# Performance work log

Measured on AMD Instinct MI355X. Metric: run time of the kernel, lower is better.

Reference implementation:

```python
import jax, jax.numpy as jnp
import numpy as np
from jax import lax

C = 256          # hidden_channels
K_ITERS = 3      # num_iterations

def _conv(x, w, b, stride=1, pad='SAME'):
    y = lax.conv_general_dilated(x, w, (stride, stride), pad,
                                 dimension_numbers=('NCHW', 'OIHW', 'NCHW'))
    return y + b[None, :, None, None]

def setup_inputs() -> dict:
    key = jax.random.key(0)
    ks = jax.random.split(key, 16)
    B, N, H, W = 1, 3, 384, 384
    def p(k, sh, scale=None):
        if scale is None:
            scale = 1.0 / np.sqrt(np.prod(sh[1:]))
        return jax.random.normal(k, sh, jnp.float32) * scale
    z = lambda: jnp.zeros((C,), jnp.float32)
    return {
        'frames': jax.random.normal(ks[0], (B, N, 3, H, W), jnp.float32),
        'backbone_w': p(ks[1], (C, 3, 8, 8)), 'backbone_b': z(),
        'W_intra': p(ks[2], (C, C), scale=1.0 / C),
        'W_inter': p(ks[3], (C, C), scale=1.0 / C),
        'gate_w': p(ks[4], (C, C, 1, 1)), 'gate_b': z(),
        'Wz': p(ks[5], (C, 2 * C, 3, 3)), 'bz': z(),
        'Wr': p(ks[6], (C, 2 * C, 3, 3)), 'br': z(),
        'Wh': p(ks[7], (C, 2 * C, 3, 3)), 'bh': z(),
        'ro_w1': p(ks[8], (C, 2 * C, 3, 3)), 'ro_b1': z(),
        'ro_w2': p(ks[9], (1, C, 3, 3)), 'ro_b2': jnp.zeros((1,), jnp.float32),
    }

def _forward(frames, backbone_w, backbone_b, W_intra, W_inter, gate_w, gate_b,
             Wz, bz, Wr, br, Wh, bh, ro_w1, ro_b1, ro_w2, ro_b2):
    B, N, _, H, W = frames.shape
    x = frames.reshape(B * N, 3, H, W)
    # backbone: stride-8 conv + ReLU -> node embeddings v (B*N, C, Hf, Wf)
    v = jax.nn.relu(_conv(x, backbone_w, backbone_b, stride=8, pad='VALID'))
    Hf, Wf = v.shape[2], v.shape[3]
    P = Hf * Wf
    v = v.reshape(B, N, C, Hf, Wf)
    h = v
    idx = jnp.arange(N)
    for _ in range(K_ITERS):
        hp = h.reshape(B, N, C, P).transpose(0, 1, 3, 2)      # (B,N,P,C)
        # inter attention e_ij = h_i W h_j^T over all ordered pairs
        t = jnp.einsum('bipc,cd->bipd', hp, W_inter)
        e = jnp.einsum('bipd,bjqd->bijpq', t, hp)              # (B,N,N,P,P)
        # intra (loop-edge) attention on the diagonal, own weight
        ti = jnp.einsum('bipc,cd->bipd', hp, W_intra)
        e_intra = jnp.einsum('bipd,biqd->bipq', ti, hp)        # (B,N,P,P)
        e = e.at[:, idx, idx].set(e_intra)
        attn = jax.nn.softmax(e, axis=-1)
        m = jnp.einsum('bijpq,bjqc->bijpc', attn, hp)          # msg j->i (B,N,N,P,C)
        m = m.transpose(0, 1, 2, 4, 3).reshape(B * N * N, C, Hf, Wf)
        # gated aggregation: sigmoid(1x1 conv) gate, sum over senders j
        g = jax.nn.sigmoid(_conv(m, gate_w, gate_b))
        magg = (g * m).reshape(B, N, N, C, Hf, Wf).sum(axis=2).reshape(B * N, C, Hf, Wf)
        # ConvGRU update
        hflat = h.reshape(B * N, C, Hf, Wf)
        mh = jnp.concatenate([magg, hflat], axis=1)
        zg = jax.nn.sigmoid(_conv(mh, Wz, bz))
        rg = jax.nn.sigmoid(_conv(mh, Wr, br))
        hc = jnp.tanh(_conv(jnp.concatenate([magg, rg * hflat], axis=1), Wh, bh))
        h = ((1.0 - zg) * hflat + zg * hc).reshape(B, N, C, Hf, Wf)
    # read-out on concat(h, v)
    cat = jnp.concatenate([h, v], axis=2).reshape(B * N, 2 * C, Hf, Wf)
    y = jax.nn.relu(_conv(cat, ro_w1, ro_b1))
    masks = _conv(y, ro_w2, ro_b2)
    return masks.reshape(B, N, 1, Hf, Wf)

def reference(frames, backbone_w, backbone_b, W_intra, W_inter, gate_w, gate_b,
              Wz, bz, Wr, br, Wh, bh, ro_w1, ro_b1, ro_w2, ro_b2):
    return _forward(frames, backbone_w, backbone_b, W_intra, W_inter, gate_w, gate_b,
                    Wz, bz, Wr, br, Wh, bh, ro_w1, ro_b1, ro_w2, ro_b2)
```

## Files before the change

### kernel.cpp

```cpp
#include <hip/hip_runtime.h>
#include <hip/hip_bf16.h>
#include <math.h>

#define PIX 2304
#define CCH 256
#define CP  589824
#define NCP 1769472
#define KC  4608
#define PADR 2512

typedef __hip_bfloat16 bf16;
typedef __attribute__((ext_vector_type(8))) short bf16x8;
typedef __attribute__((ext_vector_type(4))) float f32x4;

__device__ __forceinline__ float sigmoidf_(float x){ return 1.f/(1.f+__expf(-x)); }

__device__ __forceinline__ void gl_lds16(const bf16* g, bf16* lds){
    __builtin_amdgcn_global_load_lds(
        (const __attribute__((address_space(1))) void*)g,
        (__attribute__((address_space(3))) void*)lds, 16, 0, 0);
}
#define FENCE() asm volatile("" ::: "memory")

__device__ __forceinline__ float bperm_f(int srcLane, float v){
    return __int_as_float(__builtin_amdgcn_ds_bpermute(srcLane<<2, __float_as_int(v)));
}
__device__ __forceinline__ unsigned packbf(float lo, float hi){
    bf16 a = __float2bfloat16(lo), b = __float2bfloat16(hi);
    return (unsigned)(*(unsigned short*)&a) | ((unsigned)(*(unsigned short*)&b)<<16);
}

__global__ __launch_bounds__(512) void fattn_k(
    const bf16* __restrict__ T, const bf16* __restrict__ Ti,
    const bf16* __restrict__ Khp, const bf16* __restrict__ Vcp,
    bf16* __restrict__ Ob)
{
    __shared__ bf16 Ks[2][64*256];
    __shared__ bf16 Vs[2][256*64];
    __shared__ unsigned Ps[8][512];
    const int z = blockIdx.z, i = z/3, j = z%3;
    const bf16* Q  = ((i==j)? Ti : T) + (long)i*CP;
    const bf16* Kp = Khp + (long)j*CP;
    const bf16* Vp = Vcp + (long)j*CP;
    const int tid = threadIdx.x, l = tid & 63, w = tid >> 6;
    const int g = l>>4, m = l&15;
    const int q0 = blockIdx.x*128;

    bf16x8 qf[8];
    {
        const bf16* qr = Q + (long)(q0 + w*16 + m)*256 + g*8;
        #pragma unroll
        for (int ks=0; ks<8; ++ks) qf[ks] = *(const bf16x8*)(qr + ks*32);
    }
    f32x4 oacc[16];
    #pragma unroll
    for (int nf=0; nf<16; ++nf) oacc[nf] = (f32x4){0.f,0.f,0.f,0.f};
    float mrun = -3e38f;
    float lrun = 0.f;

    auto stage = [&](int buf, int t){
        const int kq = t*64;
        #pragma unroll
        for (int u=0; u<4; ++u){
            int idx = u*512 + tid;
            int rr = idx>>5, cc = idx&31;
            gl_lds16(Kp + (long)(kq+rr)*256 + ((cc ^ (rr&7))<<3),
                     &Ks[buf][(u*512 + (tid & ~63))*8]);
        }
        #pragma unroll
        for (int u=0; u<4; ++u){
            int idx = u*512 + tid;
            int rr = idx>>3, cc = idx&7;
            gl_lds16(Vp + (long)rr*2304 + kq + ((cc ^ (rr&7))<<3),
                     &Vs[buf][(u*512 + (tid & ~63))*8]);
        }
    };

    stage(0, 0);
    int cur = 0;
    char* pw = (char*)&Ps[w][0];
    for (int t=0; t<36; ++t){
        if (t+1 < 36){
            stage(cur^1, t+1);
            asm volatile("s_waitcnt vmcnt(8)" ::: "memory");
        } else {
            asm volatile("s_waitcnt vmcnt(0)" ::: "memory");
        }
        __builtin_amdgcn_s_barrier();
        FENCE();

        f32x4 sacc[4];
        #pragma unroll
        for (int nf=0; nf<4; ++nf) sacc[nf] = (f32x4){0.f,0.f,0.f,0.f};
        __builtin_amdgcn_s_setprio(1);
        #pragma unroll
        for (int ks=0; ks<8; ++ks){
            #pragma unroll
            for (int nf=0; nf<4; ++nf){
                int row = nf*16 + m;
                int phys = (ks*4 + g) ^ (row&7);
                bf16x8 kf = *(const bf16x8*)&Ks[cur][row*256 + phys*8];
                sacc[nf] = __builtin_amdgcn_mfma_f32_16x16x32_bf16(kf, qf[ks], sacc[nf], 0,0,0);
            }
        }
        __builtin_amdgcn_s_setprio(0);

        float pmax = -3e38f;
        #pragma unroll
        for (int nf=0; nf<4; ++nf)
            #pragma unroll
            for (int r=0; r<4; ++r) pmax = fmaxf(pmax, sacc[nf][r]);
        pmax = fmaxf(pmax, __shfl_xor(pmax, 16));
        pmax = fmaxf(pmax, __shfl_xor(pmax, 32));
        if (!__all(pmax - mrun <= 8.f)){
            float mn = fmaxf(mrun, pmax);
            float al = __expf(mrun - mn);
            mrun = mn;
            lrun *= al;
            float ar[4];
            #pragma unroll
            for (int r=0; r<4; ++r) ar[r] = bperm_f((l & 48) | (g*4 + r), al);
            #pragma unroll
            for (int nf=0; nf<16; ++nf)
                #pragma unroll
                for (int r=0; r<4; ++r) oacc[nf][r] *= ar[r];
        }
        float rs = 0.f;
        unsigned pk[4][2];
        #pragma unroll
        for (int nf=0; nf<4; ++nf){
            float p0 = __expf(sacc[nf][0] - mrun);
            float p1 = __expf(sacc[nf][1] - mrun);
            float p2 = __expf(sacc[nf][2] - mrun);
            float p3 = __expf(sacc[nf][3] - mrun);
            rs += (p0+p1) + (p2+p3);
            pk[nf][0] = packbf(p0, p1);
            pk[nf][1] = packbf(p2, p3);
        }
        rs += __shfl_xor(rs, 16);
        rs += __shfl_xor(rs, 32);
        lrun += rs;
        #pragma unroll
        for (int nf=0; nf<4; ++nf)
            #pragma unroll
            for (int s=0; s<2; ++s){
                int ba = m*128 + ((nf*32 + g*8 + s*4) ^ ((m&7)<<4));
                *(unsigned*)(pw + ba) = pk[nf][s];
            }
        asm volatile("s_waitcnt lgkmcnt(0)" ::: "memory");
        __builtin_amdgcn_sched_barrier(0);
        __builtin_amdgcn_s_setprio(1);
        #pragma unroll
        for (int ks2=0; ks2<2; ++ks2){
            bf16x8 pa = *(const bf16x8*)(pw + m*128 + ((ks2*64 + g*16) ^ ((m&7)<<4)));
            #pragma unroll
            for (int nf=0; nf<16; ++nf){
                int row = nf*16 + m;
                int phys = (ks2*4 + g) ^ (row&7);
                bf16x8 bv = *(const bf16x8*)&Vs[cur][row*64 + phys*8];
                oacc[nf] = __builtin_amdgcn_mfma_f32_16x16x32_bf16(pa, bv, oacc[nf], 0,0,0);
            }
        }
        __builtin_amdgcn_s_setprio(0);
        FENCE();
        __builtin_amdgcn_s_barrier();
        FENCE();
        cur ^= 1;
    }

    float linv = 1.f / lrun;
    float li[4];
    #pragma unroll
    for (int r=0; r<4; ++r) li[r] = bperm_f((l & 48) | (g*4 + r), linv);
    bf16* ob = Ob + (long)z*CP;
    const int prow0 = q0 + w*16 + g*4;
    #pragma unroll
    for (int nf=0; nf<16; ++nf){
        int c = nf*16 + m;
        #pragma unroll
        for (int r=0; r<4; ++r)
            ob[(long)(prow0+r)*256 + c] = __float2bfloat16(oacc[nf][r]*li[r]);
    }
}

template<int EPI, int BN>
__global__ __launch_bounds__(256) void mgemm_k(
    const bf16* __restrict__ A0, const bf16* __restrict__ A1, int diagz,
    const bf16* __restrict__ B,
    float* __restrict__ o0, bf16* __restrict__ ob,
    const bf16* __restrict__ aux, const float* __restrict__ bias0,
    int M, int N, int lda, int ldb, int ldc, int auxld,
    long bsA, long bsB, long bsC, long bsAux,
    int nzJ, int Ksub, long bsKc)
{
    __shared__ bf16 As[2][128*64];
    __shared__ bf16 Bs[2][BN*64];
    const int z = blockIdx.z;
    const int jz = z % nzJ, kc = z / nzJ;
    const bf16* Ap = ((jz==diagz)?A1:A0) + jz*bsA + (long)blockIdx.x*128*lda;
    const bf16* Bp = B + jz*bsB + (long)blockIdx.y*BN*ldb;
    const int tid = threadIdx.x, l = tid & 63;
    const int wvu = tid & ~63;
    const int wr = tid>>7, wc = (tid>>6)&1;
    constexpr int NF = BN/32;
    f32x4 acc[4][NF];
    #pragma unroll
    for (int i=0;i<4;++i)
        #pragma unroll
        for (int j=0;j<NF;++j) acc[i][j] = (f32x4){0.f,0.f,0.f,0.f};

    auto stage = [&](int buf, int kb){
        #pragma unroll
        for (int u=0;u<4;++u){
            int idx = u*256 + tid;
            int row = idx>>3, g = (idx&7) ^ (row&7);
            gl_lds16(Ap + (long)row*lda + kb + g*8, &As[buf][(u*256+wvu)*8]);
        }
        #pragma unroll
        for (int u=0;u<BN/32;++u){
            int idx = u*256 + tid;
            int row = idx>>3, g = (idx&7) ^ (row&7);
            gl_lds16(Bp + (long)row*ldb + kb + g*8, &Bs[buf][(u*256+wvu)*8]);
        }
    };

    const int kbeg = kc*Ksub;
    const int nk = Ksub >> 6;
    stage(0, kbeg);
    int cur = 0;
    for (int t=0; t<nk; ++t){
        if (t+1 < nk){
            stage(cur^1, kbeg + (t+1)*64);
            if constexpr (BN==64) asm volatile("s_waitcnt vmcnt(6)" ::: "memory");
            else                  asm volatile("s_waitcnt vmcnt(8)" ::: "memory");
        } else {
            asm volatile("s_waitcnt vmcnt(0)" ::: "memory");
        }
        __builtin_amdgcn_s_barrier();
        FENCE();
        #pragma unroll
        for (int ks=0; ks<64; ks+=32){
            bf16x8 af[4], bfr[NF];
            #pragma unroll
            for (int i=0;i<4;++i){
                int row = wr*64 + i*16 + (l&15);
                af[i] = *(const bf16x8*)&As[cur][row*64 + ((((ks>>3)+(l>>4)) ^ (row&7))<<3)];
            }
            #pragma unroll
            for (int j=0;j<NF;++j){
                int row = wc*(BN/2) + j*16 + (l&15);
                bfr[j] = *(const bf16x8*)&Bs[cur][row*64 + ((((ks>>3)+(l>>4)) ^ (row&7))<<3)];
            }
            #pragma unroll
            for (int i=0;i<4;++i)
                #pragma unroll
                for (int j=0;j<NF;++j)
                    acc[i][j] = __builtin_amdgcn_mfma_f32_16x16x32_bf16(af[i], bfr[j], acc[i][j], 0,0,0);
        }
        FENCE();
        __builtin_amdgcn_s_barrier();
        FENCE();
        cur ^= 1;
    }

    const int mb = blockIdx.x*128 + wr*64, nb = blockIdx.y*BN + wc*(BN/2);
    #pragma unroll
    for (int i=0;i<4;++i)
        #pragma unroll
        for (int j=0;j<NF;++j){
            int gm0 = mb + i*16 + ((l>>4)<<2);
            int gn  = nb + j*16 + (l&15);
            #pragma unroll
            for (int r=0;r<4;++r){
                int gm = gm0 + r;
                float vacc = acc[i][j][r];
                if (EPI==0){
                    ob[jz*bsC + (long)gm*ldc + gn] = __float2bfloat16(vacc);
                } else {
                    float g = sigmoidf_(vacc + bias0[gm]);
                    float mv = __bfloat162float(aux[jz*bsAux + (long)gn*auxld + gm]);
                    o0[jz*bsC + (long)gm*ldc + gn] = g*mv;
                }
            }
        }
}

__global__ __launch_bounds__(256) void cgemm2_k(
    const bf16* __restrict__ inpad, const bf16* __restrict__ W,
    float* __restrict__ part, int N)
{
    __shared__ bf16 As[2][128*64];
    __shared__ bf16 Bs[2][64*64];
    const int tid = threadIdx.x, l = tid & 63, wvu = tid & ~63;
    const int wr = tid>>7, wc = (tid>>6)&1;
    const int bx = blockIdx.x, by = blockIdx.y, kc = blockIdx.z;
    const int img = bx/18, m0 = (bx - img*18)*128;
    const bf16* Ab = inpad + (long)img*PADR*512;
    const bf16* Bb = W + (long)by*64*KC;
    f32x4 acc[4][2];
    #pragma unroll
    for (int i=0;i<4;++i){ acc[i][0]=(f32x4){0,0,0,0}; acc[i][1]=(f32x4){0,0,0,0}; }

    auto stageA = [&](int buf, int k0){
        int tap = k0 >> 9, ci0 = k0 & 511;
        int dy = tap/3, dx = tap - 3*dy;
        int shift = (dy-1)*50 + (dx-1);
        #pragma unroll
        for (int u=0;u<4;++u){
            int idx = u*256 + tid;
            int row = idx>>3;
            int om = m0 + row;
            int prow = om + 2*(om/48) + 51 + shift;
            int g = (idx&7) ^ (row&7);
            gl_lds16(Ab + (long)prow*512 + ci0 + g*8, &As[buf][(u*256+wvu)*8]);
        }
    };
    auto stageB = [&](int buf, int k0){
        #pragma unroll
        for (int u=0;u<2;++u){
            int idx = u*256 + tid;
            int row = idx>>3;
            int g = (idx&7) ^ (row&7);
            gl_lds16(Bb + (long)row*KC + k0 + g*8, &Bs[buf][(u*256+wvu)*8]);
        }
    };

    const int kbeg = kc*2304;
    stageA(0, kbeg); stageB(0, kbeg);
    int cur = 0;
    for (int t=0; t<36; ++t){
        if (t+1 < 36){
            stageA(cur^1, kbeg+(t+1)*64); stageB(cur^1, kbeg+(t+1)*64);
            asm volatile("s_waitcnt vmcnt(6)" ::: "memory");
        } else {
            asm volatile("s_waitcnt vmcnt(0)" ::: "memory");
        }
        __builtin_amdgcn_s_barrier();
        FENCE();
        #pragma unroll
        for (int ks=0; ks<64; ks+=32){
            bf16x8 af[4], bfr[2];
            #pragma unroll
            for (int i=0;i<4;++i){
                int row = wr*64 + i*16 + (l&15);
                af[i] = *(const bf16x8*)&As[cur][row*64 + ((((ks>>3)+(l>>4)) ^ (row&7))<<3)];
            }
            #pragma unroll
            for (int j=0;j<2;++j){
                int row = wc*32 + j*16 + (l&15);
                bfr[j] = *(const bf16x8*)&Bs[cur][row*64 + ((((ks>>3)+(l>>4)) ^ (row&7))<<3)];
            }
            #pragma unroll
            for (int i=0;i<4;++i)
                #pragma unroll
                for (int j=0;j<2;++j)
                    acc[i][j] = __builtin_amdgcn_mfma_f32_16x16x32_bf16(af[i], bfr[j], acc[i][j], 0,0,0);
        }
        FENCE();
        __builtin_amdgcn_s_barrier();
        FENCE();
        cur ^= 1;
    }

    float* pbase = part + (long)kc*N*6912 + (long)img*2304;
    #pragma unroll
    for (int i=0;i<4;++i)
        #pragma unroll
        for (int j=0;j<2;++j){
            int gm0 = m0 + wr*64 + i*16 + ((l>>4)<<2);
            int gn  = by*64 + wc*32 + j*16 + (l&15);
            *(f32x4*)&pbase[(long)gn*6912 + gm0] = acc[i][j];
        }
}

template<int ACT, int DUAL>
__global__ __launch_bounds__(256) void cred_k(const float* __restrict__ part,
        const float* __restrict__ b0, const float* __restrict__ b1,
        float* __restrict__ o0, float* __restrict__ o1,
        const float* __restrict__ hmul, int N)
{
    int id = blockIdx.x*256 + threadIdx.x;
    int c = id / 6912, g = id - c*6912;
    int img = g / 2304, p = g - img*2304;
    float v = part[id] + part[id + (long)N*6912];
    if (DUAL && c >= 256){
        int co = c - 256;
        long oidx = (long)img*CP + (long)co*PIX + p;
        o1[oidx] = sigmoidf_(v + b1[co]) * hmul[oidx];
    } else {
        float r = v + b0[c];
        if (ACT==1) r = sigmoidf_(r);
        else if (ACT==2) r = tanhf(r);
        else r = fmaxf(r, 0.f);
        o0[(long)img*CP + (long)c*PIX + p] = r;
    }
}

__global__ __launch_bounds__(256) void padtr_k(const float* __restrict__ src,
        bf16* __restrict__ dst, int cofs)
{
    __shared__ float tile[64][65];
    const int img = blockIdx.z, p0 = blockIdx.x*64, c0 = blockIdx.y*64;
    const int t = threadIdx.x, tx = t&63, tq = t>>6;
    const float* s = src + (long)img*CP;
    #pragma unroll
    for (int u=0;u<16;++u){
        int r = tq + u*4;
        tile[r][tx] = s[(long)(c0+r)*PIX + p0 + tx];
    }
    __syncthreads();
    bf16* d = dst + (long)img*PADR*512 + cofs + c0;
    #pragma unroll
    for (int u=0;u<16;++u){
        int pl = tq + u*4;
        int p = p0 + pl;
        int prow = p + 2*(p/48) + 51;
        d[(long)prow*512 + tx] = __float2bfloat16(tile[tx][pl]);
    }
}

__global__ __launch_bounds__(256) void convw_k(const float* __restrict__ src,
        bf16* __restrict__ dst, int total)
{
    int idx = blockIdx.x*256 + threadIdx.x;
    if (idx >= total) return;
    int co = idx / KC, r = idx - co*KC;
    int tap = r >> 9, ci = r & 511;
    dst[idx] = __float2bfloat16(src[(long)co*KC + ci*9 + tap]);
}

__global__ __launch_bounds__(256) void prep_h_k(const float* __restrict__ h,
        bf16* __restrict__ hcp, bf16* __restrict__ hp)
{
    __shared__ float tile[64][65];
    const int i = blockIdx.z, p0 = blockIdx.x*64, c0 = blockIdx.y*64;
    const int t = threadIdx.x, tx = t&63, tq = t>>6;
    const float* src = h + (long)i*CP;
    #pragma unroll
    for (int s=0;s<16;++s){
        int r = tq + s*4;
        float v = src[(long)(c0+r)*PIX + p0 + tx];
        tile[r][tx] = v;
        hcp[(long)i*CP + (long)(c0+r)*PIX + p0 + tx] = __float2bfloat16(v);
    }
    __syncthreads();
    #pragma unroll
    for (int s=0;s<16;++s){
        int r = tq + s*4;
        hp[(long)i*CP + (long)(p0+r)*256 + c0 + tx] = __float2bfloat16(tile[tx][r]);
    }
}

__global__ __launch_bounds__(256) void convert_w_k(const float* __restrict__ wint,
    const float* __restrict__ wintra, const float* __restrict__ gw, bf16* __restrict__ o)
{
    int t = blockIdx.x*256 + threadIdx.x;
    int d = t >> 8, c = t & 255;
    o[t]          = __float2bfloat16(wint[c*256 + d]);
    o[65536 + t]  = __float2bfloat16(wintra[c*256 + d]);
    o[131072 + t] = __float2bfloat16(gw[t]);
}

__global__ __launch_bounds__(256) void gatesum_k(const float* __restrict__ g, float* __restrict__ out)
{
    int x = blockIdx.x*256 + threadIdx.x;
    int i = blockIdx.y;
    const float* gi = g + (long)i*3*CP;
    float4 a = ((const float4*)gi)[x];
    float4 b = ((const float4*)gi)[x + CP/4];
    float4 c = ((const float4*)gi)[x + CP/2];
    float4 r; r.x=a.x+b.x+c.x; r.y=a.y+b.y+c.y; r.z=a.z+b.z+c.z; r.w=a.w+b.w+c.w;
    ((float4*)(out + (long)i*CP))[x] = r;
}

__global__ __launch_bounds__(256) void backbone_k(
    const float* __restrict__ frames, const float* __restrict__ W,
    const float* __restrict__ bias, float* __restrict__ v, float* __restrict__ h)
{
    __shared__ float wl[3*64*4];
    const int n = blockIdx.z, o0 = blockIdx.y * 4;
    const int p = blockIdx.x * 256 + threadIdx.x;
    const int y = p / 48, x = p % 48;
    for (int e = threadIdx.x; e < 768; e += 256) {
        int o_sel = e / 192, rem = e % 192, ci = rem / 64, k = rem % 64;
        wl[(ci*64 + k)*4 + o_sel] = W[((long)(o0 + o_sel)*3 + ci)*64 + k];
    }
    __syncthreads();
    float acc[4] = {0.f,0.f,0.f,0.f};
    for (int ci = 0; ci < 3; ++ci) {
        const float* src = frames + (((long)n*3 + ci)*384) * 384;
        #pragma unroll
        for (int k = 0; k < 64; ++k) {
            int ky = k >> 3, kx = k & 7;
            float iv = src[(8*y + ky)*384 + 8*x + kx];
            float4 w = ((const float4*)wl)[ci*64 + k];
            acc[0] += iv*w.x; acc[1] += iv*w.y; acc[2] += iv*w.z; acc[3] += iv*w.w;
        }
    }
    #pragma unroll
    for (int oo = 0; oo < 4; ++oo) {
        float r = fmaxf(acc[oo] + bias[o0 + oo], 0.f);
        long idx = ((long)n*CCH + o0 + oo)*PIX + p;
        v[idx] = r; h[idx] = r;
    }
}

__global__ __launch_bounds__(256) void hupd_k(const float* __restrict__ zg, const float* __restrict__ hc,
                                              float* __restrict__ h)
{
    int idx = blockIdx.x*256 + threadIdx.x;
    float z = zg[idx];
    h[idx] = (1.f - z)*h[idx] + z*hc[idx];
}

__global__ __launch_bounds__(256) void maskpart_k(const float* __restrict__ yin,
        const float* __restrict__ W, float* __restrict__ part)
{
    __shared__ float wl[288];
    const int cb = blockIdx.y * 32;
    for (int e = threadIdx.x; e < 288; e += 256) wl[e] = W[cb*9 + e];
    __syncthreads();
    int id = blockIdx.x*256 + threadIdx.x;
    int n = id / PIX, p = id - n*PIX;
    int y = p / 48, x = p % 48;
    float acc = 0.f;
    for (int ci = 0; ci < 32; ++ci) {
        const float* src = yin + ((long)n*CCH + cb + ci)*PIX;
        #pragma unroll
        for (int dy = 0; dy < 3; ++dy) {
            int yy = y + dy - 1;
            #pragma unroll
            for (int dx = 0; dx < 3; ++dx) {
                int xx = x + dx - 1;
                float iv = (yy >= 0 && yy < 48 && xx >= 0 && xx < 48) ? src[yy*48 + xx] : 0.f;
                acc += iv * wl[ci*9 + dy*3 + dx];
            }
        }
    }
    part[(long)blockIdx.y*(3*PIX) + id] = acc;
}

__global__ __launch_bounds__(256) void maskred_k(const float* __restrict__ part,
        const float* __restrict__ bias, float* __restrict__ out)
{
    int id = blockIdx.x*256 + threadIdx.x;
    float acc = bias[0];
    #pragma unroll
    for (int s = 0; s < 8; ++s) acc += part[(long)s*(3*PIX) + id];
    out[id] = acc;
}

extern "C" void kernel_launch(void* const* d_in, const int* in_sizes, int n_in,
                              void* d_out, int out_size, void* d_ws, size_t ws_size,
                              hipStream_t stream)
{
    const float* frames     = (const float*)d_in[0];
    const float* backbone_w = (const float*)d_in[1];
    const float* backbone_b = (const float*)d_in[2];
    const float* W_intra    = (const float*)d_in[3];
    const float* W_inter    = (const float*)d_in[4];
    const float* gate_w     = (const float*)d_in[5];
    const float* gate_b     = (const float*)d_in[6];
    const float* Wz         = (const float*)d_in[7];
    const float* bz         = (const float*)d_in[8];
    const float* Wr         = (const float*)d_in[9];
    const float* br         = (const float*)d_in[10];
    const float* Wh         = (const float*)d_in[11];
    const float* bh         = (const float*)d_in[12];
    const float* ro_w1      = (const float*)d_in[13];
    const float* ro_b1      = (const float*)d_in[14];
    const float* ro_w2      = (const float*)d_in[15];
    const float* ro_b2      = (const float*)d_in[16];
    float* out = (float*)d_out;
    float* ws  = (float*)d_ws;

    float* h    = ws + 0L*NCP;
    float* v    = ws + 1L*NCP;
    float* magg = ws + 2L*NCP;
    float* zg   = ws + 3L*NCP;
    float* rg   = ws + 4L*NCP;
    float* rhg  = ws + 5L*NCP;
    float* hcmb = ws + 6L*NCP;
    float* S    = ws + 7L*NCP;

    float* Mb9f   = S;
    float* hp16f  = S + 7962624;
    float* hcp16f = hp16f + 884736;
    float* t16f   = hcp16f + 884736;
    float* ti16f  = t16f + 884736;
    float* wbase  = S + 11501568;
    bf16* Wint_t   = (bf16*)wbase;
    bf16* Wintra_t = Wint_t + 65536;
    bf16* gatew16  = Wint_t + 131072;
    bf16* cw16     = (bf16*)(wbase + 98304);
    bf16* inpad    = (bf16*)(wbase + 98304 + 2359296);
    float* maskp   = wbase + 98304 + 2359296 + 1929216;

    bf16* Mb9    = (bf16*)Mb9f;
    bf16* hp16   = (bf16*)hp16f;
    bf16* hcp16  = (bf16*)hcp16f;
    bf16* t16    = (bf16*)t16f;
    bf16* ti16   = (bf16*)ti16f;
    float* hc    = hcmb;
    float* gated = zg;
    float* cpart = Mb9f;

    dim3 b256(256);

    hipMemsetAsync(inpad, 0, 3858432*sizeof(bf16), stream);
    backbone_k<<<dim3(9,64,3), b256, 0, stream>>>(frames, backbone_w, backbone_b, v, h);
    convert_w_k<<<dim3(256), b256, 0, stream>>>(W_inter, W_intra, gate_w, Wint_t);
    convw_k<<<dim3(4608), b256, 0, stream>>>(Wz, cw16, 256*KC);
    convw_k<<<dim3(4608), b256, 0, stream>>>(Wr, cw16 + 256L*KC, 256*KC);
    convw_k<<<dim3(4608), b256, 0, stream>>>(Wh, cw16 + 512L*KC, 256*KC);
    convw_k<<<dim3(4608), b256, 0, stream>>>(ro_w1, cw16 + 768L*KC, 256*KC);

    for (int it = 0; it < 3; ++it) {
        prep_h_k<<<dim3(36,4,3), b256, 0, stream>>>(h, hcp16, hp16);
        mgemm_k<0,64><<<dim3(54,4,2), b256, 0, stream>>>(hp16, hp16, -1, Wint_t,
            nullptr, t16, nullptr, nullptr,
            6912,256, 256,256,256, 0, 0L,65536L,1769472L,0L, 2, 256, 0L);
        fattn_k<<<dim3(18,1,9), dim3(512), 0, stream>>>(t16, ti16, hp16, hcp16, Mb9);
        mgemm_k<2,64><<<dim3(2,36,9), b256, 0, stream>>>(gatew16, gatew16, -1,
            Mb9, gated, nullptr, Mb9, gate_b,
            256,2304, 256,256,PIX, 256, 0L,(long)CP,(long)CP,(long)CP,
            9, 256, 0L);
        gatesum_k<<<dim3(576,3), b256, 0, stream>>>(gated, magg);
        padtr_k<<<dim3(36,4,3), b256, 0, stream>>>(magg, inpad, 0);
        padtr_k<<<dim3(36,4,3), b256, 0, stream>>>(h,    inpad, 256);
        cgemm2_k<<<dim3(54,8,2), b256, 0, stream>>>(inpad, cw16, cpart, 512);
        cred_k<1,1><<<dim3(13824), b256, 0, stream>>>(cpart, bz, br, zg, rhg, h, 512);
        padtr_k<<<dim3(36,4,3), b256, 0, stream>>>(rhg, inpad, 256);
        cgemm2_k<<<dim3(54,4,2), b256, 0, stream>>>(inpad, cw16 + 512L*KC, cpart, 256);
        cred_k<2,0><<<dim3(6912), b256, 0, stream>>>(cpart, bh, nullptr, hc, nullptr, nullptr, 256);
        hupd_k<<<dim3(6912), b256, 0, stream>>>(zg, hc, h);
    }

    padtr_k<<<dim3(36,4,3), b256, 0, stream>>>(h, inpad, 0);
    padtr_k<<<dim3(36,4,3), b256, 0, stream>>>(v, inpad, 256);
    cgemm2_k<<<dim3(54,4,2), b256, 0, stream>>>(inpad, cw16 + 768L*KC, cpart, 256);
    cred_k<3,0><<<dim3(6912), b256, 0, stream>>>(cpart, ro_b1, nullptr, zg, nullptr, nullptr, 256);
    maskpart_k<<<dim3(27,8), b256, 0, stream>>>(zg, ro_w2, maskp);
    maskred_k<<<dim3(27), b256, 0, stream>>>(maskp, ro_b2, out);
}
```

Before: 949.4 us.

## Fuse conv GEMM epilogues and drop split-K reduction kernels

Replaces the split-K implicit-GEMM 3x3 conv plus separate reduction, activation and GRU-update kernels with a single full-K GEMM kernel. Bias, sigmoid/tanh/ReLU, the r*h product and the GRU blend are applied in the epilogue. The z/r conv now uses a 128-wide N tile. This removes fp32 partial-sum traffic and several launches, but halves the grid (216 blocks, down from 432 or 864). That may underfill the GPU and lengthen each block's K loop.

Measured after the change: 1.054 ms. 1.11x slower.

```diff
diff --git a/kernel.cpp b/kernel.cpp
--- a/kernel.cpp
+++ b/kernel.cpp
@@ -285,21 +285,27 @@
         }
 }
 
-__global__ __launch_bounds__(256) void cgemm2_k(
+template<int ACT, int BN>
+__global__ __launch_bounds__(256) void cgemm3_k(
     const bf16* __restrict__ inpad, const bf16* __restrict__ W,
-    float* __restrict__ part, int N)
+    const float* __restrict__ b0, const float* __restrict__ b1,
+    float* __restrict__ o0, float* __restrict__ o1,
+    const float* __restrict__ hbuf, const float* __restrict__ zbuf)
 {
     __shared__ bf16 As[2][128*64];
-    __shared__ bf16 Bs[2][64*64];
+    __shared__ bf16 Bs[2][BN*64];
+    constexpr int NF = BN/32;
     const int tid = threadIdx.x, l = tid & 63, wvu = tid & ~63;
     const int wr = tid>>7, wc = (tid>>6)&1;
-    const int bx = blockIdx.x, by = blockIdx.y, kc = blockIdx.z;
+    const int bx = blockIdx.x, by = blockIdx.y;
     const int img = bx/18, m0 = (bx - img*18)*128;
     const bf16* Ab = inpad + (long)img*PADR*512;
-    const bf16* Bb = W + (long)by*64*KC;
-    f32x4 acc[4][2];
-    #pragma unroll
-    for (int i=0;i<4;++i){ acc[i][0]=(f32x4){0,0,0,0}; acc[i][1]=(f32x4){0,0,0,0}; }
+    const bf16* Bb = W + (long)by*BN*KC;
+    f32x4 acc[4][NF];
+    #pragma unroll
+    for (int i=0;i<4;++i)
+        #pragma unroll
+        for (int j=0;j<NF;++j) acc[i][j] = (f32x4){0.f,0.f,0.f,0.f};
 
     auto stageA = [&](int buf, int k0){
         int tap = k0 >> 9, ci0 = k0 & 511;
@@ -317,7 +323,7 @@
     };
     auto stageB = [&](int buf, int k0){
         #pragma unroll
-        for (int u=0;u<2;++u){
+        for (int u=0;u<BN/32;++u){
             int idx = u*256 + tid;
             int row = idx>>3;
             int g = (idx&7) ^ (row&7);
@@ -325,13 +331,13 @@
         }
     };
 
-    const int kbeg = kc*2304;
-    stageA(0, kbeg); stageB(0, kbeg);
+    stageA(0, 0); stageB(0, 0);
     int cur = 0;
-    for (int t=0; t<36; ++t){
-        if (t+1 < 36){
-            stageA(cur^1, kbeg+(t+1)*64); stageB(cur^1, kbeg+(t+1)*64);
-            asm volatile("s_waitcnt vmcnt(6)" ::: "memory");
+    for (int t=0; t<72; ++t){
+        if (t+1 < 72){
+            stageA(cur^1, (t+1)*64); stageB(cur^1, (t+1)*64);
+            if constexpr (BN==64) asm volatile("s_waitcnt vmcnt(6)" ::: "memory");
+            else                  asm volatile("s_waitcnt vmcnt(8)" ::: "memory");
         } else {
             asm volatile("s_waitcnt vmcnt(0)" ::: "memory");
         }
@@ -339,21 +345,21 @@
         FENCE();
         #pragma unroll
         for (int ks=0; ks<64; ks+=32){
-            bf16x8 af[4], bfr[2];
+            bf16x8 af[4], bfr[NF];
             #pragma unroll
             for (int i=0;i<4;++i){
                 int row = wr*64 + i*16 + (l&15);
                 af[i] = *(const bf16x8*)&As[cur][row*64 + ((((ks>>3)+(l>>4)) ^ (row&7))<<3)];
             }
             #pragma unroll
-            for (int j=0;j<2;++j){
-                int row = wc*32 + j*16 + (l&15);
+            for (int j=0;j<NF;++j){
+                int row = wc*(BN/2) + j*16 + (l&15);
                 bfr[j] = *(const bf16x8*)&Bs[cur][row*64 + ((((ks>>3)+(l>>4)) ^ (row&7))<<3)];
             }
             #pragma unroll
             for (int i=0;i<4;++i)
                 #pragma unroll
-                for (int j=0;j<2;++j)
+                for (int j=0;j<NF;++j)
                     acc[i][j] = __builtin_amdgcn_mfma_f32_16x16x32_bf16(af[i], bfr[j], acc[i][j], 0,0,0);
         }
         FENCE();
@@ -362,38 +368,48 @@
         cur ^= 1;
     }
 
-    float* pbase = part + (long)kc*N*6912 + (long)img*2304;
     #pragma unroll
     for (int i=0;i<4;++i)
         #pragma unroll
-        for (int j=0;j<2;++j){
+        for (int j=0;j<NF;++j){
             int gm0 = m0 + wr*64 + i*16 + ((l>>4)<<2);
-            int gn  = by*64 + wc*32 + j*16 + (l&15);
-            *(f32x4*)&pbase[(long)gn*6912 + gm0] = acc[i][j];
-        }
-}
-
-template<int ACT, int DUAL>
-__global__ __launch_bounds__(256) void cred_k(const float* __restrict__ part,
-        const float* __restrict__ b0, const float* __restrict__ b1,
-        float* __restrict__ o0, float* __restrict__ o1,
-        const float* __restrict__ hmul, int N)
-{
-    int id = blockIdx.x*256 + threadIdx.x;
-    int c = id / 6912, g = id - c*6912;
-    int img = g / 2304, p = g - img*2304;
-    float v = part[id] + part[id + (long)N*6912];
-    if (DUAL && c >= 256){
-        int co = c - 256;
-        long oidx = (long)img*CP + (long)co*PIX + p;
-        o1[oidx] = sigmoidf_(v + b1[co]) * hmul[oidx];
-    } else {
-        float r = v + b0[c];
-        if (ACT==1) r = sigmoidf_(r);
-        else if (ACT==2) r = tanhf(r);
-        else r = fmaxf(r, 0.f);
-        o0[(long)img*CP + (long)c*PIX + p] = r;
-    }
+            int gn  = by*BN + wc*(BN/2) + j*16 + (l&15);
+            f32x4 vv = acc[i][j];
+            if (ACT==1){
+                if (gn < 256){
+                    long ob = (long)img*CP + (long)gn*PIX + gm0;
+                    f32x4 r4;
+                    #pragma unroll
+                    for (int r=0;r<4;++r) r4[r] = sigmoidf_(vv[r] + b0[gn]);
+                    *(f32x4*)&o0[ob] = r4;
+                } else {
+                    int co = gn - 256;
+                    long ob = (long)img*CP + (long)co*PIX + gm0;
+                    f32x4 h4 = *(const f32x4*)&hbuf[ob];
+                    f32x4 r4;
+                    #pragma unroll
+                    for (int r=0;r<4;++r) r4[r] = sigmoidf_(vv[r] + b1[co]) * h4[r];
+                    *(f32x4*)&o1[ob] = r4;
+                }
+            } else if (ACT==2){
+                long ob = (long)img*CP + (long)gn*PIX + gm0;
+                f32x4 h4 = *(const f32x4*)&hbuf[ob];
+                f32x4 z4 = *(const f32x4*)&zbuf[ob];
+                f32x4 r4;
+                #pragma unroll
+                for (int r=0;r<4;++r){
+                    float hc = tanhf(vv[r] + b0[gn]);
+                    r4[r] = (1.f - z4[r])*h4[r] + z4[r]*hc;
+                }
+                *(f32x4*)&o0[ob] = r4;
+            } else {
+                long ob = (long)img*CP + (long)gn*PIX + gm0;
+                f32x4 r4;
+                #pragma unroll
+                for (int r=0;r<4;++r) r4[r] = fmaxf(vv[r] + b0[gn], 0.f);
+                *(f32x4*)&o0[ob] = r4;
+            }
+        }
 }
 
 __global__ __launch_bounds__(256) void padtr_k(const float* __restrict__ src,
@@ -503,14 +519,6 @@
         long idx = ((long)n*CCH + o0 + oo)*PIX + p;
         v[idx] = r; h[idx] = r;
     }
-}
-
-__global__ __launch_bounds__(256) void hupd_k(const float* __restrict__ zg, const float* __restrict__ hc,
-                                              float* __restrict__ h)
-{
-    int idx = blockIdx.x*256 + threadIdx.x;
-    float z = zg[idx];
-    h[idx] = (1.f - z)*h[idx] + z*hc[idx];
 }
 
 __global__ __launch_bounds__(256) void maskpart_k(const float* __restrict__ yin,
@@ -601,9 +609,7 @@
     bf16* hcp16  = (bf16*)hcp16f;
     bf16* t16    = (bf16*)t16f;
     bf16* ti16   = (bf16*)ti16f;
-    float* hc    = hcmb;
     float* gated = zg;
-    float* cpart = Mb9f;
 
     dim3 b256(256);
 
@@ -628,18 +634,17 @@
         gatesum_k<<<dim3(576,3), b256, 0, stream>>>(gated, magg);
         padtr_k<<<dim3(36,4,3), b256, 0, stream>>>(magg, inpad, 0);
         padtr_k<<<dim3(36,4,3), b256, 0, stream>>>(h,    inpad, 256);
-        cgemm2_k<<<dim3(54,8,2), b256, 0, stream>>>(inpad, cw16, cpart, 512);
-        cred_k<1,1><<<dim3(13824), b256, 0, stream>>>(cpart, bz, br, zg, rhg, h, 512);
+        cgemm3_k<1,128><<<dim3(54,4), b256, 0, stream>>>(inpad, cw16,
+            bz, br, zg, rhg, h, nullptr);
         padtr_k<<<dim3(36,4,3), b256, 0, stream>>>(rhg, inpad, 256);
-        cgemm2_k<<<dim3(54,4,2), b256, 0, stream>>>(inpad, cw16 + 512L*KC, cpart, 256);
-        cred_k<2,0><<<dim3(6912), b256, 0, stream>>>(cpart, bh, nullptr, hc, nullptr, nullptr, 256);
-        hupd_k<<<dim3(6912), b256, 0, stream>>>(zg, hc, h);
+        cgemm3_k<2,64><<<dim3(54,4), b256, 0, stream>>>(inpad, cw16 + 512L*KC,
+            bh, nullptr, h, nullptr, h, zg);
     }
 
     padtr_k<<<dim3(36,4,3), b256, 0, stream>>>(h, inpad, 0);
     padtr_k<<<dim3(36,4,3), b256, 0, stream>>>(v, inpad, 256);
-    cgemm2_k<<<dim3(54,4,2), b256, 0, stream>>>(inpad, cw16 + 768L*KC, cpart, 256);
-    cred_k<3,0><<<dim3(6912), b256, 0, stream>>>(cpart, ro_b1, nullptr, zg, nullptr, nullptr, 256);
+    cgemm3_k<3,64><<<dim3(54,4), b256, 0, stream>>>(inpad, cw16 + 768L*KC,
+        ro_b1, nullptr, zg, nullptr, nullptr, nullptr);
     maskpart_k<<<dim3(27,8), b256, 0, stream>>>(zg, ro_w2, maskp);
     maskred_k<<<dim3(27), b256, 0, stream>>>(maskp, ro_b2, out);
 }
```

## Fuse gate GEMM with sender sum, widen conv GEMM tile, fuse GRU update

Applied to the files above, without the earlier changes.

Adds a dedicated gate GEMM kernel that loops over the three senders in-block and accumulates sigmoid-gated messages in registers, replacing the separate gated output buffer and gatesum kernel. The conv GEMM tile grows from 64 to 128 output channels per block, halving grid size and doubling A-tile reuse but increasing registers and LDS. The candidate-state reduction and GRU update are fused into one kernel, dropping the hc buffer round trip. The generic mgemm kernel is simplified to the remaining use.

Measured after the change: 904.2 us. 4.8% less time.

```diff
diff --git a/kernel.cpp b/kernel.cpp
--- a/kernel.cpp
+++ b/kernel.cpp
@@ -183,21 +183,16 @@
     }
 }
 
-template<int EPI, int BN>
+template<int BN>
 __global__ __launch_bounds__(256) void mgemm_k(
-    const bf16* __restrict__ A0, const bf16* __restrict__ A1, int diagz,
-    const bf16* __restrict__ B,
-    float* __restrict__ o0, bf16* __restrict__ ob,
-    const bf16* __restrict__ aux, const float* __restrict__ bias0,
-    int M, int N, int lda, int ldb, int ldc, int auxld,
-    long bsA, long bsB, long bsC, long bsAux,
-    int nzJ, int Ksub, long bsKc)
+    const bf16* __restrict__ A0, const bf16* __restrict__ B, bf16* __restrict__ ob,
+    int M, int lda, int ldb, int ldc,
+    long bsB, long bsC, int nzJ, int Ksub)
 {
     __shared__ bf16 As[2][128*64];
     __shared__ bf16 Bs[2][BN*64];
-    const int z = blockIdx.z;
-    const int jz = z % nzJ, kc = z / nzJ;
-    const bf16* Ap = ((jz==diagz)?A1:A0) + jz*bsA + (long)blockIdx.x*128*lda;
+    const int jz = blockIdx.z % nzJ;
+    const bf16* Ap = A0 + (long)blockIdx.x*128*lda;
     const bf16* Bp = B + jz*bsB + (long)blockIdx.y*BN*ldb;
     const int tid = threadIdx.x, l = tid & 63;
     const int wvu = tid & ~63;
@@ -224,13 +219,12 @@
         }
     };
 
-    const int kbeg = kc*Ksub;
     const int nk = Ksub >> 6;
-    stage(0, kbeg);
+    stage(0, 0);
     int cur = 0;
     for (int t=0; t<nk; ++t){
         if (t+1 < nk){
-            stage(cur^1, kbeg + (t+1)*64);
+            stage(cur^1, (t+1)*64);
             if constexpr (BN==64) asm volatile("s_waitcnt vmcnt(6)" ::: "memory");
             else                  asm volatile("s_waitcnt vmcnt(8)" ::: "memory");
         } else {
@@ -271,17 +265,107 @@
             int gm0 = mb + i*16 + ((l>>4)<<2);
             int gn  = nb + j*16 + (l&15);
             #pragma unroll
-            for (int r=0;r<4;++r){
-                int gm = gm0 + r;
-                float vacc = acc[i][j][r];
-                if (EPI==0){
-                    ob[jz*bsC + (long)gm*ldc + gn] = __float2bfloat16(vacc);
-                } else {
-                    float g = sigmoidf_(vacc + bias0[gm]);
-                    float mv = __bfloat162float(aux[jz*bsAux + (long)gn*auxld + gm]);
-                    o0[jz*bsC + (long)gm*ldc + gn] = g*mv;
+            for (int r=0;r<4;++r)
+                ob[jz*bsC + (long)(gm0+r)*ldc + gn] = __float2bfloat16(acc[i][j][r]);
+        }
+}
+
+__global__ __launch_bounds__(256) void gatemm_k(
+    const bf16* __restrict__ gatew, const bf16* __restrict__ Mb9,
+    const float* __restrict__ gb, float* __restrict__ magg)
+{
+    __shared__ bf16 As[2][128*64];
+    __shared__ bf16 Bs[2][64*64];
+    const int tid = threadIdx.x, l = tid & 63, wvu = tid & ~63;
+    const int wr = tid>>7, wc = (tid>>6)&1;
+    const int i = blockIdx.z;
+    const bf16* Ap = gatew + (long)blockIdx.x*128*256;
+    const int nb0 = blockIdx.y*64;
+    f32x4 msum[4][2];
+    #pragma unroll
+    for (int a=0;a<4;++a){ msum[a][0]=(f32x4){0,0,0,0}; msum[a][1]=(f32x4){0,0,0,0}; }
+
+    for (int j=0; j<3; ++j){
+        const bf16* Bp = Mb9 + (long)(i*3+j)*CP + (long)nb0*256;
+        f32x4 acc[4][2];
+        #pragma unroll
+        for (int a=0;a<4;++a){ acc[a][0]=(f32x4){0,0,0,0}; acc[a][1]=(f32x4){0,0,0,0}; }
+        auto stage = [&](int buf, int kb){
+            #pragma unroll
+            for (int u=0;u<4;++u){
+                int idx = u*256 + tid;
+                int row = idx>>3, g = (idx&7) ^ (row&7);
+                gl_lds16(Ap + (long)row*256 + kb + g*8, &As[buf][(u*256+wvu)*8]);
+            }
+            #pragma unroll
+            for (int u=0;u<2;++u){
+                int idx = u*256 + tid;
+                int row = idx>>3, g = (idx&7) ^ (row&7);
+                gl_lds16(Bp + (long)row*256 + kb + g*8, &Bs[buf][(u*256+wvu)*8]);
+            }
+        };
+        stage(0, 0);
+        int cur = 0;
+        for (int t=0; t<4; ++t){
+            if (t+1 < 4){
+                stage(cur^1, (t+1)*64);
+                asm volatile("s_waitcnt vmcnt(6)" ::: "memory");
+            } else {
+                asm volatile("s_waitcnt vmcnt(0)" ::: "memory");
+            }
+            __builtin_amdgcn_s_barrier();
+            FENCE();
+            #pragma unroll
+            for (int ks=0; ks<64; ks+=32){
+                bf16x8 af[4], bfr[2];
+                #pragma unroll
+                for (int a=0;a<4;++a){
+                    int row = wr*64 + a*16 + (l&15);
+                    af[a] = *(const bf16x8*)&As[cur][row*64 + ((((ks>>3)+(l>>4)) ^ (row&7))<<3)];
                 }
-            }
+                #pragma unroll
+                for (int b=0;b<2;++b){
+                    int row = wc*32 + b*16 + (l&15);
+                    bfr[b] = *(const bf16x8*)&Bs[cur][row*64 + ((((ks>>3)+(l>>4)) ^ (row&7))<<3)];
+                }
+                #pragma unroll
+                for (int a=0;a<4;++a)
+                    #pragma unroll
+                    for (int b=0;b<2;++b)
+                        acc[a][b] = __builtin_amdgcn_mfma_f32_16x16x32_bf16(af[a], bfr[b], acc[a][b], 0,0,0);
+            }
+            FENCE();
+            __builtin_amdgcn_s_barrier();
+            FENCE();
+            cur ^= 1;
+        }
+        const bf16* mbz = Mb9 + (long)(i*3+j)*CP;
+        const int mb = blockIdx.x*128 + wr*64;
+        #pragma unroll
+        for (int a=0;a<4;++a)
+            #pragma unroll
+            for (int b=0;b<2;++b){
+                int gm0 = mb + a*16 + ((l>>4)<<2);
+                int gn  = nb0 + wc*32 + b*16 + (l&15);
+                #pragma unroll
+                for (int r=0;r<4;++r){
+                    int gm = gm0 + r;
+                    float g = sigmoidf_(acc[a][b][r] + gb[gm]);
+                    float mv = __bfloat162float(mbz[(long)gn*256 + gm]);
+                    msum[a][b][r] += g*mv;
+                }
+            }
+    }
+    const int mb = blockIdx.x*128 + wr*64;
+    #pragma unroll
+    for (int a=0;a<4;++a)
+        #pragma unroll
+        for (int b=0;b<2;++b){
+            int gm0 = mb + a*16 + ((l>>4)<<2);
+            int gn  = nb0 + wc*32 + b*16 + (l&15);
+            #pragma unroll
+            for (int r=0;r<4;++r)
+                magg[(long)i*CP + (long)(gm0+r)*PIX + gn] = msum[a][b][r];
         }
 }
 
@@ -290,16 +374,18 @@
     float* __restrict__ part, int N)
 {
     __shared__ bf16 As[2][128*64];
-    __shared__ bf16 Bs[2][64*64];
+    __shared__ bf16 Bs[2][128*64];
     const int tid = threadIdx.x, l = tid & 63, wvu = tid & ~63;
     const int wr = tid>>7, wc = (tid>>6)&1;
     const int bx = blockIdx.x, by = blockIdx.y, kc = blockIdx.z;
     const int img = bx/18, m0 = (bx - img*18)*128;
     const bf16* Ab = inpad + (long)img*PADR*512;
-    const bf16* Bb = W + (long)by*64*KC;
-    f32x4 acc[4][2];
-    #pragma unroll
-    for (int i=0;i<4;++i){ acc[i][0]=(f32x4){0,0,0,0}; acc[i][1]=(f32x4){0,0,0,0}; }
+    const bf16* Bb = W + (long)by*128*KC;
+    f32x4 acc[4][4];
+    #pragma unroll
+    for (int i=0;i<4;++i)
+        #pragma unroll
+        for (int j=0;j<4;++j) acc[i][j] = (f32x4){0.f,0.f,0.f,0.f};
 
     auto stageA = [&](int buf, int k0){
         int tap = k0 >> 9, ci0 = k0 & 511;
@@ -317,7 +403,7 @@
     };
     auto stageB = [&](int buf, int k0){
         #pragma unroll
-        for (int u=0;u<2;++u){
+        for (int u=0;u<4;++u){
             int idx = u*256 + tid;
             int row = idx>>3;
             int g = (idx&7) ^ (row&7);
@@ -331,7 +417,7 @@
     for (int t=0; t<36; ++t){
         if (t+1 < 36){
             stageA(cur^1, kbeg+(t+1)*64); stageB(cur^1, kbeg+(t+1)*64);
-            asm volatile("s_waitcnt vmcnt(6)" ::: "memory");
+            asm volatile("s_waitcnt vmcnt(8)" ::: "memory");
         } else {
             asm volatile("s_waitcnt vmcnt(0)" ::: "memory");
         }
@@ -339,21 +425,21 @@
         FENCE();
         #pragma unroll
         for (int ks=0; ks<64; ks+=32){
-            bf16x8 af[4], bfr[2];
+            bf16x8 af[4], bfr[4];
             #pragma unroll
             for (int i=0;i<4;++i){
                 int row = wr*64 + i*16 + (l&15);
                 af[i] = *(const bf16x8*)&As[cur][row*64 + ((((ks>>3)+(l>>4)) ^ (row&7))<<3)];
             }
             #pragma unroll
-            for (int j=0;j<2;++j){
-                int row = wc*32 + j*16 + (l&15);
+            for (int j=0;j<4;++j){
+                int row = wc*64 + j*16 + (l&15);
                 bfr[j] = *(const bf16x8*)&Bs[cur][row*64 + ((((ks>>3)+(l>>4)) ^ (row&7))<<3)];
             }
             #pragma unroll
             for (int i=0;i<4;++i)
                 #pragma unroll
-                for (int j=0;j<2;++j)
+                for (int j=0;j<4;++j)
                     acc[i][j] = __builtin_amdgcn_mfma_f32_16x16x32_bf16(af[i], bfr[j], acc[i][j], 0,0,0);
         }
         FENCE();
@@ -366,9 +452,9 @@
     #pragma unroll
     for (int i=0;i<4;++i)
         #pragma unroll
-        for (int j=0;j<2;++j){
+        for (int j=0;j<4;++j){
             int gm0 = m0 + wr*64 + i*16 + ((l>>4)<<2);
-            int gn  = by*64 + wc*32 + j*16 + (l&15);
+            int gn  = by*128 + wc*64 + j*16 + (l&15);
             *(f32x4*)&pbase[(long)gn*6912 + gm0] = acc[i][j];
         }
 }
@@ -396,6 +482,20 @@
     }
 }
 
+__global__ __launch_bounds__(256) void credh_k(const float* __restrict__ part,
+        const float* __restrict__ bh, const float* __restrict__ zg,
+        float* __restrict__ h)
+{
+    int id = blockIdx.x*256 + threadIdx.x;
+    int c = id / 6912, g = id - c*6912;
+    int img = g / 2304, p = g - img*2304;
+    float v = part[id] + part[id + 256L*6912];
+    float hcv = tanhf(v + bh[c]);
+    long oidx = (long)img*CP + (long)c*PIX + p;
+    float z = zg[oidx];
+    h[oidx] = (1.f - z)*h[oidx] + z*hcv;
+}
+
 __global__ __launch_bounds__(256) void padtr_k(const float* __restrict__ src,
         bf16* __restrict__ dst, int cofs)
 {
@@ -459,18 +559,6 @@
     o[t]          = __float2bfloat16(wint[c*256 + d]);
     o[65536 + t]  = __float2bfloat16(wintra[c*256 + d]);
     o[131072 + t] = __float2bfloat16(gw[t]);
-}
-
-__global__ __launch_bounds__(256) void gatesum_k(const float* __restrict__ g, float* __restrict__ out)
-{
-    int x = blockIdx.x*256 + threadIdx.x;
-    int i = blockIdx.y;
-    const float* gi = g + (long)i*3*CP;
-    float4 a = ((const float4*)gi)[x];
-    float4 b = ((const float4*)gi)[x + CP/4];
-    float4 c = ((const float4*)gi)[x + CP/2];
-    float4 r; r.x=a.x+b.x+c.x; r.y=a.y+b.y+c.y; r.z=a.z+b.z+c.z; r.w=a.w+b.w+c.w;
-    ((float4*)(out + (long)i*CP))[x] = r;
 }
 
 __global__ __launch_bounds__(256) void backbone_k(
@@ -503,14 +591,6 @@
         long idx = ((long)n*CCH + o0 + oo)*PIX + p;
         v[idx] = r; h[idx] = r;
     }
-}
-
-__global__ __launch_bounds__(256) void hupd_k(const float* __restrict__ zg, const float* __restrict__ hc,
-                                              float* __restrict__ h)
-{
-    int idx = blockIdx.x*256 + threadIdx.x;
-    float z = zg[idx];
-    h[idx] = (1.f - z)*h[idx] + z*hc[idx];
 }
 
 __global__ __launch_bounds__(256) void maskpart_k(const float* __restrict__ yin,
@@ -601,8 +681,6 @@
     bf16* hcp16  = (bf16*)hcp16f;
     bf16* t16    = (bf16*)t16f;
     bf16* ti16   = (bf16*)ti16f;
-    float* hc    = hcmb;
-    float* gated = zg;
     float* cpart = Mb9f;
 
     dim3 b256(256);
@@ -617,28 +695,22 @@
 
     for (int it = 0; it < 3; ++it) {
         prep_h_k<<<dim3(36,4,3), b256, 0, stream>>>(h, hcp16, hp16);
-        mgemm_k<0,64><<<dim3(54,4,2), b256, 0, stream>>>(hp16, hp16, -1, Wint_t,
-            nullptr, t16, nullptr, nullptr,
-            6912,256, 256,256,256, 0, 0L,65536L,1769472L,0L, 2, 256, 0L);
+        mgemm_k<64><<<dim3(54,4,2), b256, 0, stream>>>(hp16, Wint_t, t16,
+            6912, 256,256,256, 65536L, 1769472L, 2, 256);
         fattn_k<<<dim3(18,1,9), dim3(512), 0, stream>>>(t16, ti16, hp16, hcp16, Mb9);
-        mgemm_k<2,64><<<dim3(2,36,9), b256, 0, stream>>>(gatew16, gatew16, -1,
-            Mb9, gated, nullptr, Mb9, gate_b,
-            256,2304, 256,256,PIX, 256, 0L,(long)CP,(long)CP,(long)CP,
-            9, 256, 0L);
-        gatesum_k<<<dim3(576,3), b256, 0, stream>>>(gated, magg);
+        gatemm_k<<<dim3(2,36,3), b256, 0, stream>>>(gatew16, Mb9, gate_b, magg);
         padtr_k<<<dim3(36,4,3), b256, 0, stream>>>(magg, inpad, 0);
         padtr_k<<<dim3(36,4,3), b256, 0, stream>>>(h,    inpad, 256);
-        cgemm2_k<<<dim3(54,8,2), b256, 0, stream>>>(inpad, cw16, cpart, 512);
+        cgemm2_k<<<dim3(54,4,2), b256, 0, stream>>>(inpad, cw16, cpart, 512);
         cred_k<1,1><<<dim3(13824), b256, 0, stream>>>(cpart, bz, br, zg, rhg, h, 512);
         padtr_k<<<dim3(36,4,3), b256, 0, stream>>>(rhg, inpad, 256);
-        cgemm2_k<<<dim3(54,4,2), b256, 0, stream>>>(inpad, cw16 + 512L*KC, cpart, 256);
-        cred_k<2,0><<<dim3(6912), b256, 0, stream>>>(cpart, bh, nullptr, hc, nullptr, nullptr, 256);
-        hupd_k<<<dim3(6912), b256, 0, stream>>>(zg, hc, h);
+        cgemm2_k<<<dim3(54,2,2), b256, 0, stream>>>(inpad, cw16 + 512L*KC, cpart, 256);
+        credh_k<<<dim3(6912), b256, 0, stream>>>(cpart, bh, zg, h);
     }
 
     padtr_k<<<dim3(36,4,3), b256, 0, stream>>>(h, inpad, 0);
     padtr_k<<<dim3(36,4,3), b256, 0, stream>>>(v, inpad, 256);
-    cgemm2_k<<<dim3(54,4,2), b256, 0, stream>>>(inpad, cw16 + 768L*KC, cpart, 256);
+    cgemm2_k<<<dim3(54,2,2), b256, 0, stream>>>(inpad, cw16 + 768L*KC, cpart, 256);
     cred_k<3,0><<<dim3(6912), b256, 0, stream>>>(cpart, ro_b1, nullptr, zg, nullptr, nullptr, 256);
     maskpart_k<<<dim3(27,8), b256, 0, stream>>>(zg, ro_w2, maskp);
     maskred_k<<<dim3(27), b256, 0, stream>>>(maskp, ro_b2, out);
```
